# Kernel optimization log

Measured on AMD Instinct MI355X. Metric: run time of the kernel, lower is better.

The kernel has to match this reference:

```python
import jax, jax.numpy as jnp
import numpy as np

D_MODEL = 1024
N_HEADS = 16
D_K = D_MODEL // N_HEADS


def setup_inputs() -> dict:
    key = jax.random.key(0)
    ks = jax.random.split(key, 5)
    scale = 1.0 / np.sqrt(D_MODEL)
    x = jax.random.normal(ks[0], (4, 2048, D_MODEL), dtype=jnp.float32)
    W_Q = jax.random.uniform(ks[1], (D_MODEL, D_MODEL), jnp.float32, -scale, scale)
    W_K = jax.random.uniform(ks[2], (D_MODEL, D_MODEL), jnp.float32, -scale, scale)
    W_V = jax.random.uniform(ks[3], (D_MODEL, D_MODEL), jnp.float32, -scale, scale)
    W_O = jax.random.uniform(ks[4], (D_MODEL, D_MODEL), jnp.float32, -scale, scale)
    return {"x": x, "W_Q": W_Q, "W_K": W_K, "W_V": W_V, "W_O": W_O}


def reference(x, W_Q, W_K, W_V, W_O):
    B, S, _ = x.shape
    # nn.Linear(y) = y @ W.T ; weights stored (out, in)
    def heads(W):
        return jnp.einsum('bsd,ed->bse', x, W).reshape(B, S, N_HEADS, D_K).transpose(0, 2, 1, 3)
    Q, K, V = heads(W_Q), heads(W_K), heads(W_V)  # [B,H,S,Dk]
    scores = jnp.einsum('bhqd,bhkd->bhqk', Q, K) / np.sqrt(D_K)
    causal = jnp.tril(jnp.ones((S, S), dtype=bool))
    scores = jnp.where(causal[None, None], scores, -jnp.inf)
    attn = jax.nn.softmax(scores, axis=-1)  # [B,H,S,S]
    out = jnp.einsum('bhqk,bhkd->bhqd', attn, V)
    out = out.transpose(0, 2, 1, 3).reshape(B, S, D_MODEL)
    return jnp.einsum('bsd,ed->bse', out, W_O)
```

## Files before the change

kernel.cpp:

```cpp
#include <hip/hip_runtime.h>
#include <hip/hip_bf16.h>
#include <stdint.h>

#define D_MODEL 1024
#define NHEADS  16
#define DKH     64
#define BATCH   4
#define SEQ     2048
#define NTOK    (BATCH * SEQ)

typedef unsigned short u16;
using bf16x8 = __attribute__((ext_vector_type(8))) short;
using f32x4  = __attribute__((ext_vector_type(4))) float;
using f32x16 = __attribute__((ext_vector_type(16))) float;
using u32x2  = __attribute__((ext_vector_type(2))) unsigned int;

#define GLD16(g, l)                                                            \
  __builtin_amdgcn_global_load_lds(                                            \
      (const __attribute__((address_space(1))) void*)(g),                      \
      (__attribute__((address_space(3))) void*)(l), 16, 0, 0)

__device__ inline u16 f2bf(float f) {
  __hip_bfloat16 h = __float2bfloat16(f);
  return __builtin_bit_cast(u16, h);
}

__device__ inline float fexp2(float x) { return __builtin_amdgcn_exp2f(x); }

__device__ inline unsigned cvtpk(float lo, float hi) {
  unsigned r;
  asm("v_cvt_pk_bf16_f32 %0, %1, %2" : "=v"(r) : "v"(lo), "v"(hi));
  return r;
}

template <int B>
__device__ inline bf16x8 make_pfrag(const f32x16& sv) {
  unsigned x1 = cvtpk(sv[B + 0], sv[B + 1]);
  unsigned y1 = cvtpk(sv[B + 4], sv[B + 5]);
  unsigned x2 = cvtpk(sv[B + 2], sv[B + 3]);
  unsigned y2 = cvtpk(sv[B + 6], sv[B + 7]);
  u32x2 s1 = __builtin_amdgcn_permlane32_swap(x1, y1, false, false);
  u32x2 s2 = __builtin_amdgcn_permlane32_swap(x2, y2, false, false);
  union { unsigned u[4]; bf16x8 v; } r;
  r.u[0] = s1[0]; r.u[1] = s2[0]; r.u[2] = s1[1]; r.u[3] = s2[1];
  return r.v;
}

__global__ __launch_bounds__(256) void cvt_all(const float* __restrict__ x,
                                               const float* __restrict__ wq,
                                               const float* __restrict__ wk,
                                               const float* __restrict__ wv,
                                               const float* __restrict__ wo,
                                               u16* xb, u16* wqb, u16* wkb, u16* wvb, u16* wob) {
  const int XC = NTOK * D_MODEL / 4;
  const int WC = D_MODEL * D_MODEL / 4;
  const int total = XC + 4 * WC;
  for (int i = blockIdx.x * 256 + threadIdx.x; i < total; i += gridDim.x * 256) {
    const float4* s; ushort4* d; int j;
    if (i < XC)              { s = (const float4*)x;  d = (ushort4*)xb;  j = i; }
    else if (i < XC + WC)    { s = (const float4*)wq; d = (ushort4*)wqb; j = i - XC; }
    else if (i < XC + 2*WC)  { s = (const float4*)wk; d = (ushort4*)wkb; j = i - XC - WC; }
    else if (i < XC + 3*WC)  { s = (const float4*)wv; d = (ushort4*)wvb; j = i - XC - 2*WC; }
    else                     { s = (const float4*)wo; d = (ushort4*)wob; j = i - XC - 3*WC; }
    float4 v = s[j];
    d[j] = make_ushort4(f2bf(v.x), f2bf(v.y), f2bf(v.z), f2bf(v.w));
  }
}

__global__ __launch_bounds__(256) void gemm_qkv(const u16* __restrict__ A,
                                                const u16* __restrict__ Bq,
                                                const u16* __restrict__ Bk,
                                                const u16* __restrict__ Bv,
                                                u16* __restrict__ Qo,
                                                u16* __restrict__ Ko,
                                                u16* __restrict__ Vo) {
  __shared__ u16 As[128 * 64];
  __shared__ u16 Bs[128 * 64];
  const int z = blockIdx.z;
  const u16* __restrict__ Bp = z == 0 ? Bq : (z == 1 ? Bk : Bv);
  const int t = threadIdx.x, lane = t & 63, wave = t >> 6;
  const int wr = wave >> 1, wc = wave & 1;
  const int frow = lane & 15, fk = (lane >> 4) * 8;
  const int bM = blockIdx.y * 128, bN = blockIdx.x * 128;

  f32x4 acc[4][4] = {};

  for (int k0 = 0; k0 < D_MODEL; k0 += 64) {
    __syncthreads();
#pragma unroll
    for (int p = 0; p < 4; ++p) {
      int chunk = p * 256 + t;
      int r = chunk >> 3, cc = chunk & 7;
      GLD16(A + (size_t)(bM + r) * D_MODEL + k0 + cc * 8, As + (size_t)(p * 256 + (t & ~63)) * 8);
      GLD16(Bp + (size_t)(bN + r) * D_MODEL + k0 + cc * 8, Bs + (size_t)(p * 256 + (t & ~63)) * 8);
    }
    __syncthreads();

    bf16x8 a[2][4], b[2][4];
#pragma unroll
    for (int kk = 0; kk < 2; ++kk) {
#pragma unroll
      for (int m = 0; m < 4; ++m)
        a[kk][m] = *(const bf16x8*)&As[(wr * 64 + m * 16 + frow) * 64 + kk * 32 + fk];
#pragma unroll
      for (int n = 0; n < 4; ++n)
        b[kk][n] = *(const bf16x8*)&Bs[(wc * 64 + n * 16 + frow) * 64 + kk * 32 + fk];
    }
#pragma unroll
    for (int kk = 0; kk < 2; ++kk)
#pragma unroll
      for (int m = 0; m < 4; ++m)
#pragma unroll
        for (int n = 0; n < 4; ++n)
          acc[m][n] = __builtin_amdgcn_mfma_f32_16x16x32_bf16(a[kk][m], b[kk][n], acc[m][n], 0, 0, 0);
  }

  const int r0 = bM + wr * 64 + (lane >> 4) * 4;
  const int c0 = bN + wc * 64 + (lane & 15);
  if (z == 2) {
#pragma unroll
    for (int m = 0; m < 4; ++m)
#pragma unroll
      for (int n = 0; n < 4; ++n) {
        int r = r0 + m * 16;
        int cc = c0 + n * 16;
        size_t off = ((size_t)(r >> 11) * D_MODEL + cc) * SEQ + (r & (SEQ - 1));
        *(ushort4*)(Vo + off) = make_ushort4(f2bf(acc[m][n][0]), f2bf(acc[m][n][1]),
                                             f2bf(acc[m][n][2]), f2bf(acc[m][n][3]));
      }
  } else {
    u16* C = z ? Ko : Qo;
    const float sc = z ? 1.0f : 0.18033688f;
#pragma unroll
    for (int m = 0; m < 4; ++m)
#pragma unroll
      for (int n = 0; n < 4; ++n)
#pragma unroll
        for (int j = 0; j < 4; ++j)
          C[(size_t)(r0 + m * 16 + j) * D_MODEL + (c0 + n * 16)] = f2bf(acc[m][n][j] * sc);
  }
}

__global__ __launch_bounds__(256) void gemm_out(const u16* __restrict__ A,
                                                const u16* __restrict__ B,
                                                float* __restrict__ C) {
  __shared__ u16 As[128 * 64];
  __shared__ u16 Bs[128 * 64];
  const int t = threadIdx.x, lane = t & 63, wave = t >> 6;
  const int wr = wave >> 1, wc = wave & 1;
  const int frow = lane & 15, fk = (lane >> 4) * 8;
  const int bM = blockIdx.y * 128, bN = blockIdx.x * 128;

  f32x4 acc[4][4] = {};

  for (int k0 = 0; k0 < D_MODEL; k0 += 64) {
    __syncthreads();
#pragma unroll
    for (int p = 0; p < 4; ++p) {
      int chunk = p * 256 + t;
      int r = chunk >> 3, cc = chunk & 7;
      GLD16(A + (size_t)(bM + r) * D_MODEL + k0 + cc * 8, As + (size_t)(p * 256 + (t & ~63)) * 8);
      GLD16(B + (size_t)(bN + r) * D_MODEL + k0 + cc * 8, Bs + (size_t)(p * 256 + (t & ~63)) * 8);
    }
    __syncthreads();

    bf16x8 a[2][4], b[2][4];
#pragma unroll
    for (int kk = 0; kk < 2; ++kk) {
#pragma unroll
      for (int m = 0; m < 4; ++m)
        a[kk][m] = *(const bf16x8*)&As[(wr * 64 + m * 16 + frow) * 64 + kk * 32 + fk];
#pragma unroll
      for (int n = 0; n < 4; ++n)
        b[kk][n] = *(const bf16x8*)&Bs[(wc * 64 + n * 16 + frow) * 64 + kk * 32 + fk];
    }
#pragma unroll
    for (int kk = 0; kk < 2; ++kk)
#pragma unroll
      for (int m = 0; m < 4; ++m)
#pragma unroll
        for (int n = 0; n < 4; ++n)
          acc[m][n] = __builtin_amdgcn_mfma_f32_16x16x32_bf16(a[kk][m], b[kk][n], acc[m][n], 0, 0, 0);
  }

  const int r0 = bM + wr * 64 + (lane >> 4) * 4;
  const int c0 = bN + wc * 64 + (lane & 15);
#pragma unroll
  for (int m = 0; m < 4; ++m)
#pragma unroll
    for (int n = 0; n < 4; ++n)
#pragma unroll
      for (int j = 0; j < 4; ++j)
        C[(size_t)(r0 + m * 16 + j) * D_MODEL + (c0 + n * 16)] = acc[m][n][j];
}

__global__ __launch_bounds__(256) void attn_fwd(const u16* __restrict__ Q,
                                                const u16* __restrict__ K,
                                                const u16* __restrict__ Vt,
                                                u16* __restrict__ O) {
  __shared__ u16 Kl[2][64 * 64];
  __shared__ u16 Vl[2][64 * 64];
  const int t = threadIdx.x, lane = t & 63, wave = t >> 6;
  const int q = lane & 31, hi = lane >> 5;
  const int bh = blockIdx.x & 63;
  const int qtile = 15 - (blockIdx.x >> 6);
  const int q0 = qtile * 128;
  const size_t rowbase = (size_t)(bh >> 4) * SEQ;
  const int hcol = (bh & 15) * DKH;
  const size_t vbase = (size_t)bh * DKH;
  const int qw = q0 + wave * 32;
  const int nit = qtile * 2 + 2;

  auto stage = [&](int buf, int kv0) {
#pragma unroll
    for (int pp = 0; pp < 2; ++pp) {
      int chunk = pp * 256 + t;
      int r = chunk >> 3, cc = chunk & 7;
      int cs = cc ^ (r & 7);
      GLD16(K + (rowbase + kv0 + r) * D_MODEL + hcol + cs * 8,
            &Kl[buf][(size_t)(pp * 256 + (t & ~63)) * 8]);
      GLD16(Vt + (vbase + r) * SEQ + kv0 + cs * 8,
            &Vl[buf][(size_t)(pp * 256 + (t & ~63)) * 8]);
    }
  };

  stage(0, 0);

  bf16x8 qf[4];
#pragma unroll
  for (int w = 0; w < 4; ++w)
    qf[w] = *(const bf16x8*)&Q[(rowbase + qw + q) * D_MODEL + hcol + w * 16 + hi * 8];

  f32x16 ot0 = {}, ot1 = {};
  float mstate = -__builtin_inff();
  float lstate = 0.f;

  __syncthreads();
  int cur = 0;
  for (int it = 0; it < nit; ++it) {
    const int kv0 = it * 64;
    if (it + 1 < nit) stage(cur ^ 1, kv0 + 64);

    if (kv0 <= qw + 31) {
      f32x16 s0 = {}, s1 = {};
      __builtin_amdgcn_s_setprio(1);
#pragma unroll
      for (int w = 0; w < 4; ++w) {
        const int rk0 = q, rk1 = 32 + q;
        bf16x8 k0 = *(const bf16x8*)&Kl[cur][rk0 * 64 + (((2 * w + hi) ^ (rk0 & 7)) * 8)];
        bf16x8 k1 = *(const bf16x8*)&Kl[cur][rk1 * 64 + (((2 * w + hi) ^ (rk0 & 7)) * 8)];
        s0 = __builtin_amdgcn_mfma_f32_32x32x16_bf16(k0, qf[w], s0, 0, 0, 0);
        s1 = __builtin_amdgcn_mfma_f32_32x32x16_bf16(k1, qf[w], s1, 0, 0, 0);
      }
      __builtin_amdgcn_s_setprio(0);

      const int qg = qw + q;
      if (kv0 + 63 > qw) {
#pragma unroll
        for (int r = 0; r < 16; ++r) {
          const int crow = (r & 3) + 8 * (r >> 2) + 4 * hi;
          if (kv0 + crow > qg) s0[r] = -__builtin_inff();
          if (kv0 + 32 + crow > qg) s1[r] = -__builtin_inff();
        }
      }

      float pmax = fmaxf(s0[0], s0[1]);
#pragma unroll
      for (int r = 2; r < 16; ++r) pmax = fmaxf(pmax, s0[r]);
#pragma unroll
      for (int r = 0; r < 16; ++r) pmax = fmaxf(pmax, s1[r]);
      pmax = fmaxf(pmax, __shfl_xor(pmax, 32));

      if (__any(pmax > mstate + 11.5416f)) {
        float mnew = fmaxf(mstate, pmax);
        float al = fexp2(mstate - mnew);
        mstate = mnew;
        lstate *= al;
#pragma unroll
        for (int r = 0; r < 16; ++r) { ot0[r] *= al; ot1[r] *= al; }
      }
      const float mm = mstate;

      float lsum = 0.f;
#pragma unroll
      for (int r = 0; r < 16; ++r) { s0[r] = fexp2(s0[r] - mm); lsum += s0[r]; }
#pragma unroll
      for (int r = 0; r < 16; ++r) { s1[r] = fexp2(s1[r] - mm); lsum += s1[r]; }
      lsum += __shfl_xor(lsum, 32);
      lstate += lsum;

      bf16x8 pb0 = make_pfrag<0>(s0);
      bf16x8 pb1 = make_pfrag<8>(s0);
      bf16x8 pb2 = make_pfrag<0>(s1);
      bf16x8 pb3 = make_pfrag<8>(s1);

      __builtin_amdgcn_s_setprio(1);
#define PV_STEP(KB, PB)                                                                   \
      {                                                                                   \
        bf16x8 v0 = *(const bf16x8*)&Vl[cur][q * 64 + (((2 * (KB) + hi) ^ (q & 7)) * 8)]; \
        bf16x8 v1 = *(const bf16x8*)&Vl[cur][(32 + q) * 64 + (((2 * (KB) + hi) ^ (q & 7)) * 8)]; \
        ot0 = __builtin_amdgcn_mfma_f32_32x32x16_bf16(v0, PB, ot0, 0, 0, 0);              \
        ot1 = __builtin_amdgcn_mfma_f32_32x32x16_bf16(v1, PB, ot1, 0, 0, 0);              \
      }
      PV_STEP(0, pb0)
      PV_STEP(1, pb1)
      PV_STEP(2, pb2)
      PV_STEP(3, pb3)
#undef PV_STEP
      __builtin_amdgcn_s_setprio(0);
    }
    __syncthreads();
    cur ^= 1;
  }

  const float inv = 1.0f / lstate;
  u16* orow = &O[(rowbase + qw + q) * D_MODEL + hcol];
#pragma unroll
  for (int g2 = 0; g2 < 4; ++g2) {
    ushort4 a4 = make_ushort4(f2bf(ot0[4 * g2 + 0] * inv), f2bf(ot0[4 * g2 + 1] * inv),
                              f2bf(ot0[4 * g2 + 2] * inv), f2bf(ot0[4 * g2 + 3] * inv));
    *(ushort4*)&orow[8 * g2 + 4 * hi] = a4;
    ushort4 b4 = make_ushort4(f2bf(ot1[4 * g2 + 0] * inv), f2bf(ot1[4 * g2 + 1] * inv),
                              f2bf(ot1[4 * g2 + 2] * inv), f2bf(ot1[4 * g2 + 3] * inv));
    *(ushort4*)&orow[32 + 8 * g2 + 4 * hi] = b4;
  }
}

extern "C" void kernel_launch(void* const* d_in, const int* in_sizes, int n_in,
                              void* d_out, int out_size, void* d_ws, size_t ws_size,
                              hipStream_t stream) {
  const float* x  = (const float*)d_in[0];
  const float* Wq = (const float*)d_in[1];
  const float* Wk = (const float*)d_in[2];
  const float* Wv = (const float*)d_in[3];
  const float* Wo = (const float*)d_in[4];
  float* out = (float*)d_out;

  u16* ws  = (u16*)d_ws;
  u16* xb  = ws;
  u16* wqb = xb + (size_t)NTOK * D_MODEL;
  u16* wkb = wqb + (size_t)D_MODEL * D_MODEL;
  u16* wvb = wkb + (size_t)D_MODEL * D_MODEL;
  u16* wob = wvb + (size_t)D_MODEL * D_MODEL;
  u16* Qb  = wob + (size_t)D_MODEL * D_MODEL;
  u16* Kb  = Qb + (size_t)NTOK * D_MODEL;
  u16* Vb  = Kb + (size_t)NTOK * D_MODEL;
  u16* Ob  = xb;

  cvt_all<<<2048, 256, 0, stream>>>(x, Wq, Wk, Wv, Wo, xb, wqb, wkb, wvb, wob);

  gemm_qkv<<<dim3(D_MODEL / 128, NTOK / 128, 3), 256, 0, stream>>>(xb, wqb, wkb, wvb, Qb, Kb, Vb);

  attn_fwd<<<dim3(16 * 64), 256, 0, stream>>>(Qb, Kb, Vb, Ob);

  gemm_out<<<dim3(D_MODEL / 128, NTOK / 128), 256, 0, stream>>>(Ob, wob, out);
}
```

Measured before the change: 189.6 us.

## Double-buffer LDS tiles in QKV and output projection GEMMs

Both projection GEMMs now keep two LDS buffers for the A and B tiles. The next k-tile is loaded asynchronously with global_load_lds while MFMAs run on the current tile, and a single barrier per iteration replaces the previous two. The aim is to hide global-load latency behind matrix compute. In exchange, LDS use per block doubles to 64 KB, which may reduce how many blocks fit per CU.

```diff
diff --git a/kernel.cpp b/kernel.cpp
--- a/kernel.cpp
+++ b/kernel.cpp
@@ -74,8 +74,8 @@
                                                 u16* __restrict__ Qo,
                                                 u16* __restrict__ Ko,
                                                 u16* __restrict__ Vo) {
-  __shared__ u16 As[128 * 64];
-  __shared__ u16 Bs[128 * 64];
+  __shared__ u16 As[2][128 * 64];
+  __shared__ u16 Bs[2][128 * 64];
   const int z = blockIdx.z;
   const u16* __restrict__ Bp = z == 0 ? Bq : (z == 1 ? Bk : Bv);
   const int t = threadIdx.x, lane = t & 63, wave = t >> 6;
@@ -83,28 +83,33 @@
   const int frow = lane & 15, fk = (lane >> 4) * 8;
   const int bM = blockIdx.y * 128, bN = blockIdx.x * 128;
 
-  f32x4 acc[4][4] = {};
-
-  for (int k0 = 0; k0 < D_MODEL; k0 += 64) {
-    __syncthreads();
+  auto stage = [&](int buf, int k0) {
 #pragma unroll
     for (int p = 0; p < 4; ++p) {
       int chunk = p * 256 + t;
       int r = chunk >> 3, cc = chunk & 7;
-      GLD16(A + (size_t)(bM + r) * D_MODEL + k0 + cc * 8, As + (size_t)(p * 256 + (t & ~63)) * 8);
-      GLD16(Bp + (size_t)(bN + r) * D_MODEL + k0 + cc * 8, Bs + (size_t)(p * 256 + (t & ~63)) * 8);
-    }
-    __syncthreads();
+      GLD16(A + (size_t)(bM + r) * D_MODEL + k0 + cc * 8, &As[buf][(size_t)(p * 256 + (t & ~63)) * 8]);
+      GLD16(Bp + (size_t)(bN + r) * D_MODEL + k0 + cc * 8, &Bs[buf][(size_t)(p * 256 + (t & ~63)) * 8]);
+    }
+  };
+
+  f32x4 acc[4][4] = {};
+  stage(0, 0);
+  __syncthreads();
+
+  int cur = 0;
+  for (int k0 = 0; k0 < D_MODEL; k0 += 64) {
+    if (k0 + 64 < D_MODEL) stage(cur ^ 1, k0 + 64);
 
     bf16x8 a[2][4], b[2][4];
 #pragma unroll
     for (int kk = 0; kk < 2; ++kk) {
 #pragma unroll
       for (int m = 0; m < 4; ++m)
-        a[kk][m] = *(const bf16x8*)&As[(wr * 64 + m * 16 + frow) * 64 + kk * 32 + fk];
+        a[kk][m] = *(const bf16x8*)&As[cur][(wr * 64 + m * 16 + frow) * 64 + kk * 32 + fk];
 #pragma unroll
       for (int n = 0; n < 4; ++n)
-        b[kk][n] = *(const bf16x8*)&Bs[(wc * 64 + n * 16 + frow) * 64 + kk * 32 + fk];
+        b[kk][n] = *(const bf16x8*)&Bs[cur][(wc * 64 + n * 16 + frow) * 64 + kk * 32 + fk];
     }
 #pragma unroll
     for (int kk = 0; kk < 2; ++kk)
@@ -113,6 +118,9 @@
 #pragma unroll
         for (int n = 0; n < 4; ++n)
           acc[m][n] = __builtin_amdgcn_mfma_f32_16x16x32_bf16(a[kk][m], b[kk][n], acc[m][n], 0, 0, 0);
+
+    __syncthreads();
+    cur ^= 1;
   }
 
   const int r0 = bM + wr * 64 + (lane >> 4) * 4;
@@ -144,35 +152,40 @@
 __global__ __launch_bounds__(256) void gemm_out(const u16* __restrict__ A,
                                                 const u16* __restrict__ B,
                                                 float* __restrict__ C) {
-  __shared__ u16 As[128 * 64];
-  __shared__ u16 Bs[128 * 64];
+  __shared__ u16 As[2][128 * 64];
+  __shared__ u16 Bs[2][128 * 64];
   const int t = threadIdx.x, lane = t & 63, wave = t >> 6;
   const int wr = wave >> 1, wc = wave & 1;
   const int frow = lane & 15, fk = (lane >> 4) * 8;
   const int bM = blockIdx.y * 128, bN = blockIdx.x * 128;
 
-  f32x4 acc[4][4] = {};
-
-  for (int k0 = 0; k0 < D_MODEL; k0 += 64) {
-    __syncthreads();
+  auto stage = [&](int buf, int k0) {
 #pragma unroll
     for (int p = 0; p < 4; ++p) {
       int chunk = p * 256 + t;
       int r = chunk >> 3, cc = chunk & 7;
-      GLD16(A + (size_t)(bM + r) * D_MODEL + k0 + cc * 8, As + (size_t)(p * 256 + (t & ~63)) * 8);
-      GLD16(B + (size_t)(bN + r) * D_MODEL + k0 + cc * 8, Bs + (size_t)(p * 256 + (t & ~63)) * 8);
-    }
-    __syncthreads();
+      GLD16(A + (size_t)(bM + r) * D_MODEL + k0 + cc * 8, &As[buf][(size_t)(p * 256 + (t & ~63)) * 8]);
+      GLD16(B + (size_t)(bN + r) * D_MODEL + k0 + cc * 8, &Bs[buf][(size_t)(p * 256 + (t & ~63)) * 8]);
+    }
+  };
+
+  f32x4 acc[4][4] = {};
+  stage(0, 0);
+  __syncthreads();
+
+  int cur = 0;
+  for (int k0 = 0; k0 < D_MODEL; k0 += 64) {
+    if (k0 + 64 < D_MODEL) stage(cur ^ 1, k0 + 64);
 
     bf16x8 a[2][4], b[2][4];
 #pragma unroll
     for (int kk = 0; kk < 2; ++kk) {
 #pragma unroll
       for (int m = 0; m < 4; ++m)
-        a[kk][m] = *(const bf16x8*)&As[(wr * 64 + m * 16 + frow) * 64 + kk * 32 + fk];
+        a[kk][m] = *(const bf16x8*)&As[cur][(wr * 64 + m * 16 + frow) * 64 + kk * 32 + fk];
 #pragma unroll
       for (int n = 0; n < 4; ++n)
-        b[kk][n] = *(const bf16x8*)&Bs[(wc * 64 + n * 16 + frow) * 64 + kk * 32 + fk];
+        b[kk][n] = *(const bf16x8*)&Bs[cur][(wc * 64 + n * 16 + frow) * 64 + kk * 32 + fk];
     }
 #pragma unroll
     for (int kk = 0; kk < 2; ++kk)
@@ -181,6 +194,9 @@
 #pragma unroll
         for (int n = 0; n < 4; ++n)
           acc[m][n] = __builtin_amdgcn_mfma_f32_16x16x32_bf16(a[kk][m], b[kk][n], acc[m][n], 0, 0, 0);
+
+    __syncthreads();
+    cur ^= 1;
   }
 
   const int r0 = bM + wr * 64 + (lane >> 4) * 4;
```

After: 185.3 us. 1.02x faster.
